# Performance work log

Measured on AMD Instinct MI355X. Metric: run time of the kernel, lower is better.

Reference implementation:

```python
import jax, jax.numpy as jnp
import numpy as np

N_NODES = 100000
N_EDGES = 1600000
EMBED_DIM = 128
HIDDEN_DIM = 256


def setup_inputs() -> dict:
    key = jax.random.key(0)
    k_emb, k_src, k_dst, k_w1, k_w2 = jax.random.split(key, 5)
    emb = jax.random.normal(k_emb, (N_NODES, EMBED_DIM), dtype=jnp.float32)
    edge_src = jax.random.randint(k_src, (N_EDGES,), 0, N_NODES)
    edge_dst = jax.random.randint(k_dst, (N_EDGES,), 0, N_NODES)
    # Linear(2D -> H) and Linear(H -> D), stored as [in, out] for x @ W
    W1 = jax.random.normal(k_w1, (2 * EMBED_DIM, HIDDEN_DIM), dtype=jnp.float32) * (1.0 / np.sqrt(2 * EMBED_DIM))
    b1 = jnp.zeros((HIDDEN_DIM,), dtype=jnp.float32)
    W2 = jax.random.normal(k_w2, (HIDDEN_DIM, EMBED_DIM), dtype=jnp.float32) * (1.0 / np.sqrt(HIDDEN_DIM))
    b2 = jnp.zeros((EMBED_DIM,), dtype=jnp.float32)
    return {"emb": emb, "edge_src": edge_src, "edge_dst": edge_dst,
            "W1": W1, "b1": b1, "W2": W2, "b2": b2}


def reference(emb, edge_src, edge_dst, W1, b1, W2, b2):
    N, D = emb.shape
    E = edge_src.shape[0]
    # gather neighbor embeddings and segment-mean per destination node
    gathered = emb[edge_src]                                    # [E, D]
    nbr_sum = jax.ops.segment_sum(gathered, edge_dst, num_segments=N)   # [N, D]
    counts = jax.ops.segment_sum(jnp.ones((E,), emb.dtype), edge_dst, num_segments=N)  # [N]
    nbr_mean = nbr_sum / jnp.maximum(counts, 1.0)[:, None]
    # nodes with no neighbors fall back to their own embedding
    nbr_mean = jnp.where(counts[:, None] == 0, emb, nbr_mean)
    concat = jnp.concatenate([emb, nbr_mean], axis=-1)          # [N, 2D]
    h = jax.nn.relu(concat @ W1 + b1)                           # [N, H]
    return h @ W2 + b2                                          # [N, D]
```

## Files before the change

### kernel.cpp

```cpp
#include <hip/hip_runtime.h>

#define DD 128
#define HH 256
#define K1 256
#define BM 64
#define CH 2048
#define CHP 8192
#define CAP 8192

typedef __bf16 bf16;
typedef __attribute__((ext_vector_type(8))) __bf16 bf16x8;
typedef __attribute__((ext_vector_type(4))) float f32x4;
typedef __attribute__((ext_vector_type(2))) float f32x2;


__global__ __launch_bounds__(256) void countb_k(const int* __restrict__ dst,
                                                int* __restrict__ bcnt,
                                                int E, int BSH) {
    __shared__ int c[512];
    for (int j = threadIdx.x; j < 512; j += 256) c[j] = 0;
    __syncthreads();
    for (int e = blockIdx.x * 256 + threadIdx.x; e < E; e += gridDim.x * 256)
        atomicAdd(&c[dst[e] >> BSH], 1);
    __syncthreads();
    for (int j = threadIdx.x; j < 512; j += 256)
        if (c[j]) atomicAdd(&bcnt[j], c[j]);
}

__global__ __launch_bounds__(512) void scanb_k(const int* __restrict__ bcnt,
                                               int* __restrict__ bbase,
                                               int* __restrict__ bpos,
                                               int NB, int E) {
    __shared__ int s[512];
    const int t = threadIdx.x;
    int v = (t < NB) ? bcnt[t] : 0;
    s[t] = v;
    __syncthreads();
    for (int off = 1; off < 512; off <<= 1) {
        int y = (t >= off) ? s[t - off] : 0;
        __syncthreads();
        s[t] += y;
        __syncthreads();
    }
    int excl = s[t] - v;
    if (t < NB) { bbase[t] = excl; bpos[t] = excl; }
    if (t == 0) bbase[NB] = E;
}

__global__ __launch_bounds__(256) void part_k(const int* __restrict__ src,
                                              const int* __restrict__ dst,
                                              int* __restrict__ bpos,
                                              unsigned* __restrict__ pairs,
                                              int E, int BSH, int Bm1) {
    __shared__ int lcnt[512];
    __shared__ int lpref[512];
    __shared__ int lrun[512];
    __shared__ int gbase[512];
    __shared__ unsigned stage[CHP];
    const int t = threadIdx.x;
    const int e0 = blockIdx.x * CHP;
    const int e1 = min(E, e0 + CHP);
    for (int j = t; j < 512; j += 256) lcnt[j] = 0;
    __syncthreads();
    for (int e = e0 + t; e < e1; e += 256)
        atomicAdd(&lcnt[dst[e] >> BSH], 1);
    __syncthreads();
    for (int j = t; j < 512; j += 256) lpref[j] = lcnt[j];
    __syncthreads();
    for (int off = 1; off < 512; off <<= 1) {
        int j2 = t + 256;
        int v0 = (t >= off) ? lpref[t - off] : 0;
        int v1 = (j2 >= off) ? lpref[j2 - off] : 0;
        __syncthreads();
        lpref[t] += v0;
        lpref[j2] += v1;
        __syncthreads();
    }
    for (int j = t; j < 512; j += 256) {
        int c = lcnt[j];
        gbase[j] = c ? atomicAdd(&bpos[j], c) : 0;
        lrun[j] = lpref[j] - c;
    }
    __syncthreads();
    for (int e = e0 + t; e < e1; e += 256) {
        int d = dst[e];
        int b = d >> BSH;
        int pos = atomicAdd(&lrun[b], 1);
        stage[pos] = ((unsigned)(d & Bm1) << 24) | (unsigned)src[e];
    }
    __syncthreads();
    const int wv = t >> 6, ln = t & 63;
    for (int b = wv; b < 512; b += 4) {
        int s = lpref[b] - lcnt[b];
        int c = lcnt[b];
        int g = gbase[b];
        for (int i = ln; i < c; i += 64)
            pairs[g + i] = stage[s + i];
    }
}

__global__ __launch_bounds__(256) void sortb_k(const unsigned* __restrict__ pairs,
                                               const int* __restrict__ bbase,
                                               int* __restrict__ offs,
                                               int* __restrict__ ssrc,
                                               int N, int BSH) {
    __shared__ int hist[512];
    __shared__ int pref[512];
    __shared__ int run[512];
    __shared__ int sorted[CAP];
    const int t = threadIdx.x;
    const int b = blockIdx.x;
    const int B = 1 << BSH;
    const int d0 = b << BSH;
    const int nd = min(B, N - d0);
    const int rb = bbase[b], re = bbase[b + 1];
    const int cntE = re - rb;
    for (int j = t; j < 512; j += 256) hist[j] = 0;
    __syncthreads();
    for (int i = rb + t; i < re; i += 256)
        atomicAdd(&hist[pairs[i] >> 24], 1);
    __syncthreads();
    for (int j = t; j < 512; j += 256) pref[j] = hist[j];
    __syncthreads();
    for (int off = 1; off < 512; off <<= 1) {
        int j2 = t + 256;
        int v0 = (t >= off) ? pref[t - off] : 0;
        int v1 = (j2 >= off) ? pref[j2 - off] : 0;
        __syncthreads();
        pref[t] += v0;
        pref[j2] += v1;
        __syncthreads();
    }
    for (int j = t; j < nd; j += 256) offs[d0 + j] = rb + pref[j];
    for (int j = t; j < 512; j += 256) run[j] = pref[j] - hist[j];
    __syncthreads();
    if (cntE <= CAP) {
        for (int i = rb + t; i < re; i += 256) {
            unsigned p = pairs[i];
            int pos = atomicAdd(&run[p >> 24], 1);
            sorted[pos] = (int)(p & 0xFFFFFFu);
        }
        __syncthreads();
        for (int i = t; i < cntE; i += 256) ssrc[rb + i] = sorted[i];
    } else {
        for (int i = rb + t; i < re; i += 256) {
            unsigned p = pairs[i];
            int pos = atomicAdd(&run[p >> 24], 1);
            ssrc[rb + pos] = (int)(p & 0xFFFFFFu);
        }
    }
}


__global__ __launch_bounds__(256) void hist_k(const int* __restrict__ dst,
                                              int* __restrict__ cnt, int E) {
    for (int e = blockIdx.x * blockDim.x + threadIdx.x; e < E;
         e += gridDim.x * blockDim.x)
        atomicAdd(&cnt[dst[e]], 1);
}

__global__ __launch_bounds__(256) void scan1_k(const int* __restrict__ cnt,
                                               int* __restrict__ offs,
                                               int* __restrict__ part, int N) {
    __shared__ int sdata[256];
    const int b = blockIdx.x, t = threadIdx.x;
    const int base = b * 1024 + t * 4;
    int v[4], sum = 0;
    #pragma unroll
    for (int i = 0; i < 4; ++i) {
        int idx = base + i;
        v[i] = (idx < N) ? cnt[idx] : 0;
        sum += v[i];
    }
    sdata[t] = sum;
    __syncthreads();
    for (int off = 1; off < 256; off <<= 1) {
        int y = (t >= off) ? sdata[t - off] : 0;
        __syncthreads();
        sdata[t] += y;
        __syncthreads();
    }
    int excl = sdata[t] - sum;
    if (t == 255) part[b] = sdata[255];
    int run = excl;
    #pragma unroll
    for (int i = 0; i < 4; ++i) {
        int idx = base + i;
        if (idx < N) offs[idx] = run;
        run += v[i];
    }
}

__global__ __launch_bounds__(128) void scan2_k(int* __restrict__ part, int nparts) {
    __shared__ int sdata[128];
    const int t = threadIdx.x;
    int v = (t < nparts) ? part[t] : 0;
    sdata[t] = v;
    __syncthreads();
    for (int off = 1; off < 128; off <<= 1) {
        int y = (t >= off) ? sdata[t - off] : 0;
        __syncthreads();
        sdata[t] += y;
        __syncthreads();
    }
    if (t < nparts) part[t] = sdata[t] - v;
}

__global__ __launch_bounds__(256) void scan3_k(int* __restrict__ offs,
                                               const int* __restrict__ part, int N) {
    for (int i = blockIdx.x * blockDim.x + threadIdx.x; i < N;
         i += gridDim.x * blockDim.x)
        offs[i] += part[i >> 10];
}

__global__ __launch_bounds__(256) void bucket_k(const int* __restrict__ src,
                                                const int* __restrict__ dst,
                                                int* __restrict__ offs,
                                                int* __restrict__ ssrc,
                                                int E, int N) {
    const int r = blockIdx.x & 7;
    const int chunk = blockIdx.x >> 3;
    const int lo = r * (N >> 3);
    const int hi = (r == 7) ? N : lo + (N >> 3);
    const int e0 = chunk * CH;
    const int e1 = min(E, e0 + CH);
    for (int e = e0 + threadIdx.x; e < e1; e += 256) {
        int d = dst[e];
        if (d >= lo && d < hi) {
            int pos = atomicAdd(&offs[d], 1);
            ssrc[pos] = src[e];
        }
    }
}

__global__ __launch_bounds__(256) void gather_k(const float* __restrict__ emb,
                                                const int* __restrict__ offs,
                                                const int* __restrict__ ssrc,
                                                float* __restrict__ nbr, int N) {
    const int wid = threadIdx.x >> 6;
    const int lane = threadIdx.x & 63;
    const int d = blockIdx.x * 4 + wid;
    if (d >= N) return;
    const int sub = lane >> 5;
    const int c = (lane & 31) * 4;
    const int start = (d == 0) ? 0 : offs[d - 1];
    const int end = offs[d];
    float4 acc = make_float4(0.f, 0.f, 0.f, 0.f);
    int e = start;
    for (; e + 4 <= end; e += 4) {
        int s0 = ssrc[e + sub];
        int s1 = ssrc[e + 2 + sub];
        float4 v0 = *reinterpret_cast<const float4*>(&emb[(size_t)s0 * DD + c]);
        float4 v1 = *reinterpret_cast<const float4*>(&emb[(size_t)s1 * DD + c]);
        acc.x += v0.x + v1.x; acc.y += v0.y + v1.y;
        acc.z += v0.z + v1.z; acc.w += v0.w + v1.w;
    }
    for (; e + 2 <= end; e += 2) {
        int s = ssrc[e + sub];
        float4 v = *reinterpret_cast<const float4*>(&emb[(size_t)s * DD + c]);
        acc.x += v.x; acc.y += v.y; acc.z += v.z; acc.w += v.w;
    }
    if (e < end && sub == 0) {
        int s = ssrc[e];
        float4 v = *reinterpret_cast<const float4*>(&emb[(size_t)s * DD + c]);
        acc.x += v.x; acc.y += v.y; acc.z += v.z; acc.w += v.w;
    }
    acc.x += __shfl_xor(acc.x, 32);
    acc.y += __shfl_xor(acc.y, 32);
    acc.z += __shfl_xor(acc.z, 32);
    acc.w += __shfl_xor(acc.w, 32);
    if (sub == 0) {
        if (end > start) {
            float inv = 1.f / (float)(end - start);
            acc.x *= inv; acc.y *= inv; acc.z *= inv; acc.w *= inv;
        } else {
            acc = *reinterpret_cast<const float4*>(&emb[(size_t)d * DD + c]);
        }
        *reinterpret_cast<float4*>(&nbr[(size_t)d * DD + c]) = acc;
    }
}

__global__ __launch_bounds__(256) void cvt8_k(const float* __restrict__ emb,
                                              unsigned* __restrict__ emb8,
                                              size_t n8) {
    for (size_t i = blockIdx.x * blockDim.x + threadIdx.x; i < n8;
         i += (size_t)gridDim.x * blockDim.x) {
        float4 a = *reinterpret_cast<const float4*>(&emb[i * 8]);
        float4 b = *reinterpret_cast<const float4*>(&emb[i * 8 + 4]);
        int w0 = __builtin_amdgcn_cvt_pk_fp8_f32(a.x, a.y, 0, false);
        w0 = __builtin_amdgcn_cvt_pk_fp8_f32(a.z, a.w, w0, true);
        int w1 = __builtin_amdgcn_cvt_pk_fp8_f32(b.x, b.y, 0, false);
        w1 = __builtin_amdgcn_cvt_pk_fp8_f32(b.z, b.w, w1, true);
        uint2 o; o.x = (unsigned)w0; o.y = (unsigned)w1;
        *reinterpret_cast<uint2*>(&emb8[i * 2]) = o;
    }
}

__device__ __forceinline__ void acc8(float* acc, uint2 v) {
    f32x2 p;
    p = __builtin_amdgcn_cvt_pk_f32_fp8(v.x, false); acc[0] += p[0]; acc[1] += p[1];
    p = __builtin_amdgcn_cvt_pk_f32_fp8(v.x, true);  acc[2] += p[0]; acc[3] += p[1];
    p = __builtin_amdgcn_cvt_pk_f32_fp8(v.y, false); acc[4] += p[0]; acc[5] += p[1];
    p = __builtin_amdgcn_cvt_pk_f32_fp8(v.y, true);  acc[6] += p[0]; acc[7] += p[1];
}

__global__ __launch_bounds__(256) void gather8_k(const unsigned* __restrict__ emb8,
                                                 const float* __restrict__ emb,
                                                 const int* __restrict__ offs,
                                                 const int* __restrict__ ssrc,
                                                 bf16* __restrict__ nbrh, int N) {
    const int wid = threadIdx.x >> 6;
    const int lane = threadIdx.x & 63;
    const int d = blockIdx.x * 4 + wid;
    if (d >= N) return;
    const int slot = lane >> 4;
    const int c8 = (lane & 15) * 8;
    const int start = (d == 0) ? 0 : offs[d - 1];
    const int end = offs[d];
    float acc[8];
    #pragma unroll
    for (int j = 0; j < 8; ++j) acc[j] = 0.f;
    int e = start;
    for (; e + 16 <= end; e += 16) {
        int s0 = ssrc[e + slot];
        int s1 = ssrc[e + 4 + slot];
        int s2 = ssrc[e + 8 + slot];
        int s3 = ssrc[e + 12 + slot];
        uint2 v0 = *reinterpret_cast<const uint2*>(&emb8[((size_t)s0 * DD + c8) >> 2]);
        uint2 v1 = *reinterpret_cast<const uint2*>(&emb8[((size_t)s1 * DD + c8) >> 2]);
        uint2 v2 = *reinterpret_cast<const uint2*>(&emb8[((size_t)s2 * DD + c8) >> 2]);
        uint2 v3 = *reinterpret_cast<const uint2*>(&emb8[((size_t)s3 * DD + c8) >> 2]);
        acc8(acc, v0); acc8(acc, v1); acc8(acc, v2); acc8(acc, v3);
    }
    for (; e + 8 <= end; e += 8) {
        int s0 = ssrc[e + slot];
        int s1 = ssrc[e + 4 + slot];
        uint2 v0 = *reinterpret_cast<const uint2*>(&emb8[((size_t)s0 * DD + c8) >> 2]);
        uint2 v1 = *reinterpret_cast<const uint2*>(&emb8[((size_t)s1 * DD + c8) >> 2]);
        acc8(acc, v0); acc8(acc, v1);
    }
    for (; e + 4 <= end; e += 4) {
        int s0 = ssrc[e + slot];
        uint2 v0 = *reinterpret_cast<const uint2*>(&emb8[((size_t)s0 * DD + c8) >> 2]);
        acc8(acc, v0);
    }
    if (slot < end - e) {
        int s0 = ssrc[e + slot];
        uint2 v0 = *reinterpret_cast<const uint2*>(&emb8[((size_t)s0 * DD + c8) >> 2]);
        acc8(acc, v0);
    }
    #pragma unroll
    for (int j = 0; j < 8; ++j) {
        acc[j] += __shfl_xor(acc[j], 16);
        acc[j] += __shfl_xor(acc[j], 32);
    }
    if (slot == 0) {
        bf16x8 o;
        if (end > start) {
            float inv = 1.f / (float)(end - start);
            #pragma unroll
            for (int j = 0; j < 8; ++j) o[j] = (bf16)(acc[j] * inv);
        } else {
            float4 a = *reinterpret_cast<const float4*>(&emb[(size_t)d * DD + c8]);
            float4 b = *reinterpret_cast<const float4*>(&emb[(size_t)d * DD + c8 + 4]);
            o[0]=(bf16)a.x; o[1]=(bf16)a.y; o[2]=(bf16)a.z; o[3]=(bf16)a.w;
            o[4]=(bf16)b.x; o[5]=(bf16)b.y; o[6]=(bf16)b.z; o[7]=(bf16)b.w;
        }
        *reinterpret_cast<bf16x8*>(&nbrh[(size_t)d * DD + c8]) = o;
    }
}

__global__ __launch_bounds__(64) void packW_k(const float* __restrict__ W1,
                                              const float* __restrict__ W2,
                                              bf16* __restrict__ w1h,
                                              bf16* __restrict__ w2h) {
    const int bid = blockIdx.x;
    const float* W; bf16* outp; int NC; int rel;
    if (bid < 128) { W = W1; outp = w1h; NC = HH; rel = bid; }
    else           { W = W2; outp = w2h; NC = DD; rel = bid - 128; }
    const int ntiles = NC >> 4;
    const int kt = rel / ntiles;
    const int nt = rel % ntiles;
    const int l = threadIdx.x;
    const int k0 = kt * 32 + (l >> 4) * 8;
    const int n = nt * 16 + (l & 15);
    bf16x8 hv;
    #pragma unroll
    for (int r = 0; r < 8; ++r)
        hv[r] = (bf16)W[(size_t)(k0 + r) * NC + n];
    *reinterpret_cast<bf16x8*>(outp + ((size_t)rel * 64 + l) * 8) = hv;
}

__global__ __launch_bounds__(512) void mlp_mfma_k(const float* __restrict__ emb,
        const float* nbrf, const bf16* __restrict__ nbrh,
        const bf16* __restrict__ w1h, const float* __restrict__ b1,
        const bf16* __restrict__ w2h, const float* __restrict__ b2,
        float* out, int N) {
    __shared__ char smem[BM * K1 * 2];
    const int t = threadIdx.x;
    const int n0 = blockIdx.x * BM;
    const int l = t & 63;
    const int w = t >> 6;

    #pragma unroll
    for (int i = 0; i < 4; ++i) {
        int chunk = i * 512 + t;
        int row = chunk >> 5;
        int c0 = (chunk & 31) * 8;
        int n = n0 + row;
        bf16x8 hv;
        if (n < N) {
            if (c0 >= DD && nbrh != nullptr) {
                hv = *reinterpret_cast<const bf16x8*>(&nbrh[(size_t)n * DD + (c0 - DD)]);
            } else {
                const float* sp = (c0 < DD) ? &emb[(size_t)n * DD + c0]
                                            : &nbrf[(size_t)n * DD + (c0 - DD)];
                float4 a = *reinterpret_cast<const float4*>(sp);
                float4 b = *reinterpret_cast<const float4*>(sp + 4);
                hv[0]=(bf16)a.x; hv[1]=(bf16)a.y; hv[2]=(bf16)a.z; hv[3]=(bf16)a.w;
                hv[4]=(bf16)b.x; hv[5]=(bf16)b.y; hv[6]=(bf16)b.z; hv[7]=(bf16)b.w;
            }
        } else {
            #pragma unroll
            for (int j = 0; j < 8; ++j) hv[j] = (bf16)0.f;
        }
        int off = row * 512 + ((c0 * 2) ^ ((row & 7) << 4));
        *reinterpret_cast<bf16x8*>(smem + off) = hv;
    }
    __syncthreads();

    const int arow = l & 15;
    const int abyte = (l >> 4) * 16;

    f32x4 acc[4][2];
    #pragma unroll
    for (int ntl = 0; ntl < 2; ++ntl) {
        float bv = b1[w * 32 + ntl * 16 + (l & 15)];
        #pragma unroll
        for (int mt = 0; mt < 4; ++mt)
            acc[mt][ntl] = (f32x4){bv, bv, bv, bv};
    }
    for (int kt = 0; kt < 8; ++kt) {
        bf16x8 ah[4];
        #pragma unroll
        for (int mt = 0; mt < 4; ++mt) {
            int row = mt * 16 + arow;
            int off = row * 512 + ((kt * 64 + abyte) ^ ((row & 7) << 4));
            ah[mt] = *reinterpret_cast<const bf16x8*>(smem + off);
        }
        #pragma unroll
        for (int ntl = 0; ntl < 2; ++ntl) {
            int nt = w * 2 + ntl;
            size_t boff = ((size_t)(kt * 16 + nt) * 64 + l) * 8;
            bf16x8 bh = *reinterpret_cast<const bf16x8*>(w1h + boff);
            #pragma unroll
            for (int mt = 0; mt < 4; ++mt)
                acc[mt][ntl] = __builtin_amdgcn_mfma_f32_16x16x32_bf16(ah[mt], bh, acc[mt][ntl], 0, 0, 0);
        }
    }
    __syncthreads();

    #pragma unroll
    for (int mt = 0; mt < 4; ++mt)
        #pragma unroll
        for (int ntl = 0; ntl < 2; ++ntl) {
            int col = w * 32 + ntl * 16 + (l & 15);
            #pragma unroll
            for (int r = 0; r < 4; ++r) {
                int row = mt * 16 + (l >> 4) * 4 + r;
                int off = row * 512 + ((col * 2) ^ ((row & 7) << 4));
                *reinterpret_cast<bf16*>(smem + off) = (bf16)fmaxf(acc[mt][ntl][r], 0.f);
            }
        }
    __syncthreads();

    f32x4 acc2[4];
    {
        float bv = b2[w * 16 + (l & 15)];
        #pragma unroll
        for (int mt = 0; mt < 4; ++mt)
            acc2[mt] = (f32x4){bv, bv, bv, bv};
    }
    for (int kt = 0; kt < 8; ++kt) {
        bf16x8 ah[4];
        #pragma unroll
        for (int mt = 0; mt < 4; ++mt) {
            int row = mt * 16 + arow;
            int off = row * 512 + ((kt * 64 + abyte) ^ ((row & 7) << 4));
            ah[mt] = *reinterpret_cast<const bf16x8*>(smem + off);
        }
        size_t boff = ((size_t)(kt * 8 + w) * 64 + l) * 8;
        bf16x8 bh = *reinterpret_cast<const bf16x8*>(w2h + boff);
        #pragma unroll
        for (int mt = 0; mt < 4; ++mt)
            acc2[mt] = __builtin_amdgcn_mfma_f32_16x16x32_bf16(ah[mt], bh, acc2[mt], 0, 0, 0);
    }
    #pragma unroll
    for (int mt = 0; mt < 4; ++mt) {
        int col = w * 16 + (l & 15);
        #pragma unroll
        for (int r = 0; r < 4; ++r) {
            int row = mt * 16 + (l >> 4) * 4 + r;
            int n = n0 + row;
            if (n < N) out[(size_t)n * DD + col] = acc2[mt][r];
        }
    }
}

__global__ __launch_bounds__(256) void scatter_k(const float* __restrict__ emb,
        const int* __restrict__ src, const int* __restrict__ dst,
        float* nbr, float* __restrict__ cnt, int E) {
    int e = blockIdx.x * 8 + (threadIdx.x >> 5);
    if (e >= E) return;
    int lane = threadIdx.x & 31;
    int s = src[e];
    int d = dst[e];
    const float4 v = *reinterpret_cast<const float4*>(&emb[(size_t)s * DD + lane * 4]);
    float* o = &nbr[(size_t)d * DD + lane * 4];
    atomicAdd(o + 0, v.x);
    atomicAdd(o + 1, v.y);
    atomicAdd(o + 2, v.z);
    atomicAdd(o + 3, v.w);
    if (lane == 0) atomicAdd(&cnt[d], 1.0f);
}

__global__ __launch_bounds__(256) void mlp_k(const float* __restrict__ emb,
        const float* nbr, const float* cnt,
        const float* __restrict__ W1, const float* __restrict__ b1,
        const float* __restrict__ W2, const float* __restrict__ b2,
        float* out, int N) {
    __shared__ float smem[BM * K1];
    const int t = threadIdx.x;
    const int n0 = blockIdx.x * BM;
    #pragma unroll
    for (int it = 0; it < 16; ++it) {
        int idx = it * 256 + t;
        int r = idx >> 6;
        int c4 = idx & 63;
        int n = n0 + r;
        float4 v = make_float4(0.f, 0.f, 0.f, 0.f);
        if (n < N) {
            if (c4 < 32) {
                v = *reinterpret_cast<const float4*>(&emb[(size_t)n * DD + c4 * 4]);
            } else {
                float c = cnt[n];
                if (c > 0.f) {
                    v = *reinterpret_cast<const float4*>(&nbr[(size_t)n * DD + (c4 - 32) * 4]);
                    float inv = 1.f / c;
                    v.x *= inv; v.y *= inv; v.z *= inv; v.w *= inv;
                } else {
                    v = *reinterpret_cast<const float4*>(&emb[(size_t)n * DD + (c4 - 32) * 4]);
                }
            }
        }
        *reinterpret_cast<float4*>(&smem[idx * 4]) = v;
    }
    __syncthreads();
    const int tx = t & 31;
    const int ty = t >> 5;
    const int r0 = ty * 8;
    {
        const int c0 = tx * 8;
        float acc[8][8];
        const float4 bva = *reinterpret_cast<const float4*>(&b1[c0]);
        const float4 bvb = *reinterpret_cast<const float4*>(&b1[c0 + 4]);
        #pragma unroll
        for (int i = 0; i < 8; ++i) {
            acc[i][0] = bva.x; acc[i][1] = bva.y; acc[i][2] = bva.z; acc[i][3] = bva.w;
            acc[i][4] = bvb.x; acc[i][5] = bvb.y; acc[i][6] = bvb.z; acc[i][7] = bvb.w;
        }
        for (int k0 = 0; k0 < K1; k0 += 4) {
            float xs[8][4];
            #pragma unroll
            for (int i = 0; i < 8; ++i) {
                float4 xv = *reinterpret_cast<const float4*>(&smem[(r0 + i) * K1 + k0]);
                xs[i][0] = xv.x; xs[i][1] = xv.y; xs[i][2] = xv.z; xs[i][3] = xv.w;
            }
            #pragma unroll
            for (int kk = 0; kk < 4; ++kk) {
                const float4 wa = *reinterpret_cast<const float4*>(&W1[(size_t)(k0 + kk) * HH + c0]);
                const float4 wb = *reinterpret_cast<const float4*>(&W1[(size_t)(k0 + kk) * HH + c0 + 4]);
                #pragma unroll
                for (int i = 0; i < 8; ++i) {
                    float x = xs[i][kk];
                    acc[i][0] += x * wa.x; acc[i][1] += x * wa.y;
                    acc[i][2] += x * wa.z; acc[i][3] += x * wa.w;
                    acc[i][4] += x * wb.x; acc[i][5] += x * wb.y;
                    acc[i][6] += x * wb.z; acc[i][7] += x * wb.w;
                }
            }
        }
        __syncthreads();
        #pragma unroll
        for (int i = 0; i < 8; ++i) {
            float4 h0, h1;
            h0.x = fmaxf(acc[i][0], 0.f); h0.y = fmaxf(acc[i][1], 0.f);
            h0.z = fmaxf(acc[i][2], 0.f); h0.w = fmaxf(acc[i][3], 0.f);
            h1.x = fmaxf(acc[i][4], 0.f); h1.y = fmaxf(acc[i][5], 0.f);
            h1.z = fmaxf(acc[i][6], 0.f); h1.w = fmaxf(acc[i][7], 0.f);
            *reinterpret_cast<float4*>(&smem[(r0 + i) * HH + c0]) = h0;
            *reinterpret_cast<float4*>(&smem[(r0 + i) * HH + c0 + 4]) = h1;
        }
        __syncthreads();
    }
    {
        const int c0 = tx * 4;
        float acc[8][4];
        const float4 bv = *reinterpret_cast<const float4*>(&b2[c0]);
        #pragma unroll
        for (int i = 0; i < 8; ++i) {
            acc[i][0] = bv.x; acc[i][1] = bv.y; acc[i][2] = bv.z; acc[i][3] = bv.w;
        }
        for (int k0 = 0; k0 < HH; k0 += 4) {
            float hs[8][4];
            #pragma unroll
            for (int i = 0; i < 8; ++i) {
                float4 hv = *reinterpret_cast<const float4*>(&smem[(r0 + i) * HH + k0]);
                hs[i][0] = hv.x; hs[i][1] = hv.y; hs[i][2] = hv.z; hs[i][3] = hv.w;
            }
            #pragma unroll
            for (int kk = 0; kk < 4; ++kk) {
                const float4 w2 = *reinterpret_cast<const float4*>(&W2[(size_t)(k0 + kk) * DD + c0]);
                #pragma unroll
                for (int i = 0; i < 8; ++i) {
                    float h = hs[i][kk];
                    acc[i][0] += h * w2.x; acc[i][1] += h * w2.y;
                    acc[i][2] += h * w2.z; acc[i][3] += h * w2.w;
                }
            }
        }
        #pragma unroll
        for (int i = 0; i < 8; ++i) {
            int n = n0 + r0 + i;
            if (n < N) {
                float4 o;
                o.x = acc[i][0]; o.y = acc[i][1]; o.z = acc[i][2]; o.w = acc[i][3];
                *reinterpret_cast<float4*>(&out[(size_t)n * DD + c0]) = o;
            }
        }
    }
}

extern "C" void kernel_launch(void* const* d_in, const int* in_sizes, int n_in,
                              void* d_out, int out_size, void* d_ws, size_t ws_size,
                              hipStream_t stream) {
    const float* emb = (const float*)d_in[0];
    const int* esrc  = (const int*)d_in[1];
    const int* edst  = (const int*)d_in[2];
    const float* W1  = (const float*)d_in[3];
    const float* b1  = (const float*)d_in[4];
    const float* W2  = (const float*)d_in[5];
    const float* b2  = (const float*)d_in[6];
    float* out = (float*)d_out;

    const int N = in_sizes[0] / DD;
    const int E = in_sizes[1];
    const int nparts = (N + 1023) / 1024;

    int BSH = 0;
    while ((((size_t)N + ((size_t)1 << BSH) - 1) >> BSH) > 512) ++BSH;
    const int B = 1 << BSH;
    const int NB = (N + B - 1) >> BSH;

    int* cnt  = (int*)d_ws;
    int* offs = cnt + N;
    int* part = offs + N;
    int* aux  = part + 128;
    int* ssrc = aux + 2048;
    char* wp = (char*)(ssrc + E);
    wp = (char*)(((uintptr_t)wp + 15) & ~(uintptr_t)15);
    bf16* w1h = (bf16*)wp;
    bf16* w2h = w1h + 65536;
    unsigned* emb8 = (unsigned*)(w2h + 32768);
    bf16* nbrh = (bf16*)(emb8 + (size_t)N * DD / 4);
    unsigned* pairs = emb8;
    int* bcnt  = aux;
    int* bbase = aux + 512;
    int* bpos  = aux + 1280;
    const size_t need_base = (size_t)((char*)(w2h + 32768) - (char*)d_ws);
    const size_t need_full = (size_t)((char*)(nbrh + (size_t)N * DD) - (char*)d_ws);
    const bool pairs_fit = ((size_t)E * 4 <= (size_t)N * DD);

    if (ws_size >= need_base && nparts <= 128) {
        const bool fast = (ws_size >= need_full) && pairs_fit && (BSH <= 8) &&
                          (N < (1 << 24)) && ((N & 7) == 0) && (NB <= 512);
        packW_k<<<dim3(192), dim3(64), 0, stream>>>(W1, W2, w1h, w2h);
        if (fast) {
            hipMemsetAsync(bcnt, 0, 512 * sizeof(int), stream);
            countb_k<<<dim3(512), dim3(256), 0, stream>>>(edst, bcnt, E, BSH);
            scanb_k<<<dim3(1), dim3(512), 0, stream>>>(bcnt, bbase, bpos, NB, E);
            part_k<<<dim3((E + CHP - 1) / CHP), dim3(256), 0, stream>>>(
                esrc, edst, bpos, pairs, E, BSH, B - 1);
            sortb_k<<<dim3(NB), dim3(256), 0, stream>>>(pairs, bbase, offs, ssrc, N, BSH);
            cvt8_k<<<dim3(2048), dim3(256), 0, stream>>>(emb, emb8, (size_t)N * DD / 8);
            gather8_k<<<dim3((N + 3) / 4), dim3(256), 0, stream>>>(emb8, emb, offs, ssrc, nbrh, N);
            mlp_mfma_k<<<dim3((N + BM - 1) / BM), dim3(512), 0, stream>>>(
                emb, nullptr, nbrh, w1h, b1, w2h, b2, out, N);
        } else {
            hipMemsetAsync(cnt, 0, (size_t)N * sizeof(int), stream);
            hist_k<<<dim3(1024), dim3(256), 0, stream>>>(edst, cnt, E);
            scan1_k<<<dim3(nparts), dim3(256), 0, stream>>>(cnt, offs, part, N);
            scan2_k<<<dim3(1), dim3(128), 0, stream>>>(part, nparts);
            scan3_k<<<dim3(512), dim3(256), 0, stream>>>(offs, part, N);
            const int nchunks = (E + CH - 1) / CH;
            bucket_k<<<dim3(nchunks * 8), dim3(256), 0, stream>>>(esrc, edst, offs, ssrc, E, N);
            gather_k<<<dim3((N + 3) / 4), dim3(256), 0, stream>>>(emb, offs, ssrc, out, N);
            mlp_mfma_k<<<dim3((N + BM - 1) / BM), dim3(512), 0, stream>>>(
                emb, out, nullptr, w1h, b1, w2h, b2, out, N);
        }
    } else {
        float* fcnt = (float*)d_ws;
        hipMemsetAsync(out, 0, (size_t)N * DD * sizeof(float), stream);
        hipMemsetAsync(fcnt, 0, (size_t)N * sizeof(float), stream);
        scatter_k<<<dim3((E + 7) / 8), dim3(256), 0, stream>>>(emb, esrc, edst, out, fcnt, E);
        mlp_k<<<dim3((N + BM - 1) / BM), dim3(256), 0, stream>>>(
            emb, out, fcnt, W1, b1, W2, b2, out, N);
    }
}
```

Before: 177.4 us.

## Simplify bucket partition kernel to direct scatter without LDS staging

Reworks the edge partition kernel to drop the per-block prefix scan and the 32KB LDS staging buffer. Bucket ids are now cached in registers and each edge is written straight to its global slot via a shared-memory atomic counter. The chunk per block is halved so more blocks run and LDS use per block falls. The cost is scattered, uncoalesced global writes in place of the coalesced per-bucket copy-out, and dst is read twice from global memory.

```diff
diff --git a/kernel.cpp b/kernel.cpp
--- a/kernel.cpp
+++ b/kernel.cpp
@@ -5,7 +5,7 @@
 #define K1 256
 #define BM 64
 #define CH 2048
-#define CHP 8192
+#define CH1 4096
 #define CAP 8192
 
 typedef __bf16 bf16;
@@ -53,49 +53,35 @@
                                               unsigned* __restrict__ pairs,
                                               int E, int BSH, int Bm1) {
     __shared__ int lcnt[512];
-    __shared__ int lpref[512];
-    __shared__ int lrun[512];
-    __shared__ int gbase[512];
-    __shared__ unsigned stage[CHP];
+    __shared__ int lbase[512];
     const int t = threadIdx.x;
-    const int e0 = blockIdx.x * CHP;
-    const int e1 = min(E, e0 + CHP);
+    const int e0 = blockIdx.x * CH1;
+    const int e1 = min(E, e0 + CH1);
     for (int j = t; j < 512; j += 256) lcnt[j] = 0;
     __syncthreads();
-    for (int e = e0 + t; e < e1; e += 256)
-        atomicAdd(&lcnt[dst[e] >> BSH], 1);
-    __syncthreads();
-    for (int j = t; j < 512; j += 256) lpref[j] = lcnt[j];
-    __syncthreads();
-    for (int off = 1; off < 512; off <<= 1) {
-        int j2 = t + 256;
-        int v0 = (t >= off) ? lpref[t - off] : 0;
-        int v1 = (j2 >= off) ? lpref[j2 - off] : 0;
-        __syncthreads();
-        lpref[t] += v0;
-        lpref[j2] += v1;
-        __syncthreads();
-    }
+    int rs[CH1 / 256];
+    #pragma unroll
+    for (int k = 0; k < CH1 / 256; ++k) {
+        int e = e0 + k * 256 + t;
+        int b = -1;
+        if (e < e1) { b = dst[e] >> BSH; atomicAdd(&lcnt[b], 1); }
+        rs[k] = b;
+    }
+    __syncthreads();
     for (int j = t; j < 512; j += 256) {
         int c = lcnt[j];
-        gbase[j] = c ? atomicAdd(&bpos[j], c) : 0;
-        lrun[j] = lpref[j] - c;
-    }
-    __syncthreads();
-    for (int e = e0 + t; e < e1; e += 256) {
-        int d = dst[e];
-        int b = d >> BSH;
-        int pos = atomicAdd(&lrun[b], 1);
-        stage[pos] = ((unsigned)(d & Bm1) << 24) | (unsigned)src[e];
-    }
-    __syncthreads();
-    const int wv = t >> 6, ln = t & 63;
-    for (int b = wv; b < 512; b += 4) {
-        int s = lpref[b] - lcnt[b];
-        int c = lcnt[b];
-        int g = gbase[b];
-        for (int i = ln; i < c; i += 64)
-            pairs[g + i] = stage[s + i];
+        lbase[j] = c ? atomicAdd(&bpos[j], c) : 0;
+        lcnt[j] = 0;
+    }
+    __syncthreads();
+    #pragma unroll
+    for (int k = 0; k < CH1 / 256; ++k) {
+        int e = e0 + k * 256 + t;
+        if (e < e1) {
+            int b = rs[k];
+            int slot = lbase[b] + atomicAdd(&lcnt[b], 1);
+            pairs[slot] = ((unsigned)(dst[e] & Bm1) << 24) | (unsigned)src[e];
+        }
     }
 }
 
@@ -689,7 +675,7 @@
             hipMemsetAsync(bcnt, 0, 512 * sizeof(int), stream);
             countb_k<<<dim3(512), dim3(256), 0, stream>>>(edst, bcnt, E, BSH);
             scanb_k<<<dim3(1), dim3(512), 0, stream>>>(bcnt, bbase, bpos, NB, E);
-            part_k<<<dim3((E + CHP - 1) / CHP), dim3(256), 0, stream>>>(
+            part_k<<<dim3((E + CH1 - 1) / CH1), dim3(256), 0, stream>>>(
                 esrc, edst, bpos, pairs, E, BSH, B - 1);
             sortb_k<<<dim3(NB), dim3(256), 0, stream>>>(pairs, bbase, offs, ssrc, N, BSH);
             cvt8_k<<<dim3(2048), dim3(256), 0, stream>>>(emb, emb8, (size_t)N * DD / 8);
```

New measurement: 153.9 us. -13.3%, faster.
